# Kernel tuning notes

Hardware: AMD Instinct MI355X
Metric: run time of the kernel (lower is better)

## Reference

```python
import jax, jax.numpy as jnp
import numpy as np
import math

RCR = 5.2
ETAR = np.array([16.0], dtype=np.float32)
SHFR = np.array([0.9, 1.16875, 1.4375, 1.70625, 1.975, 2.24375, 2.5125, 2.78125,
                 3.05, 3.31875, 3.5875, 3.85625, 4.125, 4.39375, 4.6625, 4.93125],
                dtype=np.float32)
# cartesian product of (EtaR, ShfR) -> [P, 2], P = 1*16 = 16
_PAIRS = np.stack(np.meshgrid(ETAR, SHFR, indexing='ij'), axis=-1).reshape(-1, 2)
ETA_P = jnp.asarray(_PAIRS[:, 0])  # [P]
SHF_P = jnp.asarray(_PAIRS[:, 1])  # [P]


def setup_inputs() -> dict:
    key = jax.random.key(0)
    k1, k2 = jax.random.split(key)
    B, N = 16, 512
    d = jax.random.uniform(k1, (B, N, N), dtype=jnp.float32, minval=0.0, maxval=10.0)
    d = 0.5 * (d + jnp.transpose(d, (0, 2, 1)))          # symmetric distances
    d = d * (1.0 - jnp.eye(N, dtype=jnp.float32))        # zero diagonal (self-distance)
    z = jax.random.randint(k2, (B, N), 1, 10).astype(jnp.float32)
    return {"distance_matrices": d, "atomic_numbers_batch": z}


def reference(distance_matrices, atomic_numbers_batch):
    d = distance_matrices                                  # [B, N, N]  (i, j)
    # cutoff mask: within Rcr and not the zero self/padding entries
    mask = (d < RCR) & (d != 0.0)                          # [B, N, N]
    fc = 0.5 * jnp.cos(math.pi * d / RCR) + 0.5            # [B, N, N]
    z_j = atomic_numbers_batch[:, None, :]                 # [B, 1, N]
    # radial term per (pair, param): z_j * exp(-eta*(R-shf)^2) * fC(R)
    g = jnp.exp(-ETA_P * (d[..., None] - SHF_P) ** 2)      # [B, N, N, P]
    addends = (z_j * fc)[..., None] * g                    # [B, N, N, P]
    addends = jnp.where(mask[..., None], addends, 0.0)
    # sum over neighbors j (equivalent to the scatter-into-ragged + reduce_sum)
    GR_batch = jnp.sum(addends, axis=2)                    # [B, N, P]
    return GR_batch
```

## Files before the change

### kernel.cpp

```cpp
#include <hip/hip_runtime.h>

#ifndef __has_builtin
#define __has_builtin(x) 0
#endif

__device__ __forceinline__ float fexp2(float x) {
#if __has_builtin(__builtin_amdgcn_exp2f)
    return __builtin_amdgcn_exp2f(x);
#else
    return exp2f(x);
#endif
}

__device__ __forceinline__ float fcos_rev(float r) {
#if __has_builtin(__builtin_amdgcn_cosf)
    return __builtin_amdgcn_cosf(r);
#else
    return __cosf(r * 6.283185307179586f);
#endif
}

constexpr int NATOMS = 512;
constexpr int NP     = 16;


__device__ __forceinline__ void process_elem(float dv, float zv, float* acc,
                                             float k2, float cwh, float cvh) {
    const float C   = -23.083120654223414f;
    const float A   = 12.407177351645085f;
    const float B   = -1.6672144566f;
    const float REV = 0.09615384615384616f;

    bool  valid = (dv < 5.2f) && (dv != 0.0f);
    float fc    = fmaf(0.5f, fcos_rev(dv * REV), 0.5f);
    float we    = valid ? zv * fc : 0.0f;

    float tl = dv - 1.975f;
    float th = dv - 4.125f;
    float gl = we * fexp2((C * tl) * tl);
    float gh = we * fexp2((C * th) * th);
    float wl = fexp2(fmaf(A, tl, B));
    float vl = fexp2(fmaf(-A, tl, B));
    float wh = wl * cwh;
    float vh = vl * cvh;

    acc[4] += gl;
    float g = gl * wl; acc[5] += g; wl *= k2;
    g = g * wl;        acc[6] += g; wl *= k2;
    g = g * wl;        acc[7] += g;
    g = gl * vl;       acc[3] += g; vl *= k2;
    g = g * vl;        acc[2] += g; vl *= k2;
    g = g * vl;        acc[1] += g; vl *= k2;
    g = g * vl;        acc[0] += g;

    acc[12] += gh;
    g = gh * wh;       acc[13] += g; wh *= k2;
    g = g * wh;        acc[14] += g; wh *= k2;
    g = g * wh;        acc[15] += g;
    g = gh * vh;       acc[11] += g; vh *= k2;
    g = g * vh;        acc[10] += g; vh *= k2;
    g = g * vh;        acc[9]  += g; vh *= k2;
    g = g * vh;        acc[8]  += g;
}

__global__ __launch_bounds__(256, 4) void aev_radial_kernel(
        const float* __restrict__ d,
        const float* __restrict__ z,
        float* __restrict__ out)
{
    const int lane = threadIdx.x & 63;
    const int wave = threadIdx.x >> 6;
    const int row  = blockIdx.x * 4 + wave;
    const int b    = row >> 9;

    const float4* __restrict__ dd = reinterpret_cast<const float4*>(d + (size_t)row * NATOMS);
    const float4* __restrict__ zz = reinterpret_cast<const float4*>(z + (size_t)b   * NATOMS);

    const float k2  = fexp2(-3.3344289132f);
    const float cwh = fexp2(-26.675431306f);
    const float cvh = fexp2( 26.675431306f);

    float acc[NP];
#pragma unroll
    for (int p = 0; p < NP; ++p) acc[p] = 0.0f;

#pragma unroll
    for (int h = 0; h < 2; ++h) {
        float4 dv4 = dd[lane + 64 * h];
        float4 zv4 = zz[lane + 64 * h];
        process_elem(dv4.x, zv4.x, acc, k2, cwh, cvh);
        process_elem(dv4.y, zv4.y, acc, k2, cwh, cvh);
        process_elem(dv4.z, zv4.z, acc, k2, cwh, cvh);
        process_elem(dv4.w, zv4.w, acc, k2, cwh, cvh);
    }

    bool u;
    float r0[8];
    u = (lane & 1) != 0;
#pragma unroll
    for (int k = 0; k < 8; ++k) {
        float snd  = u ? acc[k] : acc[k + 8];
        float rcv  = __shfl_xor(snd, 1, 64);
        float kept = u ? acc[k + 8] : acc[k];
        r0[k] = kept + rcv;
    }
    float r1[4];
    u = (lane & 2) != 0;
#pragma unroll
    for (int k = 0; k < 4; ++k) {
        float snd  = u ? r1[0] : r1[0];
        (void)snd;
        float s2   = u ? r0[k] : r0[k + 4];
        float rcv  = __shfl_xor(s2, 2, 64);
        float kept = u ? r0[k + 4] : r0[k];
        r1[k] = kept + rcv;
    }
    float r2[2];
    u = (lane & 4) != 0;
#pragma unroll
    for (int k = 0; k < 2; ++k) {
        float s2   = u ? r1[k] : r1[k + 2];
        float rcv  = __shfl_xor(s2, 4, 64);
        float kept = u ? r1[k + 2] : r1[k];
        r2[k] = kept + rcv;
    }
    float r3;
    u = (lane & 8) != 0;
    {
        float s2   = u ? r2[0] : r2[1];
        float rcv  = __shfl_xor(s2, 8, 64);
        float kept = u ? r2[1] : r2[0];
        r3 = kept + rcv;
    }
    r3 += __shfl_xor(r3, 16, 64);
    r3 += __shfl_xor(r3, 32, 64);

    int idx = ((lane & 1) << 3) | ((lane & 2) << 1) | ((lane & 4) >> 1) | ((lane & 8) >> 3);
    if (lane < 16) {
        out[(size_t)row * NP + idx] = r3;
    }
}

extern "C" void kernel_launch(void* const* d_in, const int* in_sizes, int n_in,
                              void* d_out, int out_size, void* d_ws, size_t ws_size,
                              hipStream_t stream) {
    const float* d  = (const float*)d_in[0];
    const float* z  = (const float*)d_in[1];
    float* out      = (float*)d_out;

    aev_radial_kernel<<<dim3(2048), dim3(256), 0, stream>>>(d, z, out);
}
```

Before: 69.06 us.

## Compact in-cutoff neighbors into LDS before evaluating radial terms

Each wave first ballots which neighbor distances fall inside the cutoff and stream-compacts their (distance, Z) pairs into a per-wave shared-memory buffer. It then runs the exp/cos radial evaluation only over the compacted list in 64-lane rounds, padding the tail with zero-weight entries. This skips transcendental work for out-of-cutoff pairs. The cost is extra LDS traffic, ballot/mbcnt overhead, a data-dependent loop and 16 KB of shared memory per block.

Measured after the change: 69.22 us. Within noise of the previous version (+0.2%).

```diff
diff --git a/kernel.cpp b/kernel.cpp
--- a/kernel.cpp
+++ b/kernel.cpp
@@ -31,9 +31,8 @@
     const float B   = -1.6672144566f;
     const float REV = 0.09615384615384616f;
 
-    bool  valid = (dv < 5.2f) && (dv != 0.0f);
-    float fc    = fmaf(0.5f, fcos_rev(dv * REV), 0.5f);
-    float we    = valid ? zv * fc : 0.0f;
+    float fc = fmaf(0.5f, fcos_rev(dv * REV), 0.5f);
+    float we = zv * fc;
 
     float tl = dv - 1.975f;
     float th = dv - 4.125f;
@@ -76,22 +75,47 @@
     const float4* __restrict__ dd = reinterpret_cast<const float4*>(d + (size_t)row * NATOMS);
     const float4* __restrict__ zz = reinterpret_cast<const float4*>(z + (size_t)b   * NATOMS);
 
+    __shared__ float2 buf[4][NATOMS];
+    float2* __restrict__ wbuf = buf[wave];
+
     const float k2  = fexp2(-3.3344289132f);
     const float cwh = fexp2(-26.675431306f);
     const float cvh = fexp2( 26.675431306f);
+
+    unsigned int cnt = 0;
+#pragma unroll
+    for (int h = 0; h < 2; ++h) {
+        float4 dv4 = dd[lane + 64 * h];
+        float4 zv4 = zz[lane + 64 * h];
+#pragma unroll
+        for (int q = 0; q < 4; ++q) {
+            float dv = (&dv4.x)[q];
+            float zv = (&zv4.x)[q];
+            bool valid = (dv < 5.2f) && (dv != 0.0f);
+            unsigned long long bal = __ballot(valid);
+            unsigned int lo = (unsigned int)(bal & 0xffffffffull);
+            unsigned int hi = (unsigned int)(bal >> 32);
+            unsigned int prefix = __builtin_amdgcn_mbcnt_hi(hi,
+                                    __builtin_amdgcn_mbcnt_lo(lo, 0));
+            if (valid) {
+                wbuf[cnt + prefix] = make_float2(dv, zv);
+            }
+            cnt += (unsigned int)__popcll(bal);
+        }
+    }
 
     float acc[NP];
 #pragma unroll
     for (int p = 0; p < NP; ++p) acc[p] = 0.0f;
 
-#pragma unroll
-    for (int h = 0; h < 2; ++h) {
-        float4 dv4 = dd[lane + 64 * h];
-        float4 zv4 = zz[lane + 64 * h];
-        process_elem(dv4.x, zv4.x, acc, k2, cwh, cvh);
-        process_elem(dv4.y, zv4.y, acc, k2, cwh, cvh);
-        process_elem(dv4.z, zv4.z, acc, k2, cwh, cvh);
-        process_elem(dv4.w, zv4.w, acc, k2, cwh, cvh);
+    const unsigned int rounds = (cnt + 63u) >> 6;
+    for (unsigned int r = 0; r < rounds; ++r) {
+        unsigned int idx = (r << 6) + lane;
+        float2 e = wbuf[idx];
+        bool ok  = idx < cnt;
+        float dv = ok ? e.x : 3.0f;
+        float zv = ok ? e.y : 0.0f;
+        process_elem(dv, zv, acc, k2, cwh, cvh);
     }
 
     bool u;
@@ -108,10 +132,8 @@
     u = (lane & 2) != 0;
 #pragma unroll
     for (int k = 0; k < 4; ++k) {
-        float snd  = u ? r1[0] : r1[0];
-        (void)snd;
-        float s2   = u ? r0[k] : r0[k + 4];
-        float rcv  = __shfl_xor(s2, 2, 64);
+        float snd  = u ? r0[k] : r0[k + 4];
+        float rcv  = __shfl_xor(snd, 2, 64);
         float kept = u ? r0[k + 4] : r0[k];
         r1[k] = kept + rcv;
     }
@@ -119,16 +141,16 @@
     u = (lane & 4) != 0;
 #pragma unroll
     for (int k = 0; k < 2; ++k) {
-        float s2   = u ? r1[k] : r1[k + 2];
-        float rcv  = __shfl_xor(s2, 4, 64);
+        float snd  = u ? r1[k] : r1[k + 2];
+        float rcv  = __shfl_xor(snd, 4, 64);
         float kept = u ? r1[k + 2] : r1[k];
         r2[k] = kept + rcv;
     }
     float r3;
     u = (lane & 8) != 0;
     {
-        float s2   = u ? r2[0] : r2[1];
-        float rcv  = __shfl_xor(s2, 8, 64);
+        float snd  = u ? r2[0] : r2[1];
+        float rcv  = __shfl_xor(snd, 8, 64);
         float kept = u ? r2[1] : r2[0];
         r3 = kept + rcv;
     }
```
